# Optimization experiments

Measured on AMD Instinct MI355X. Metric: run time of the kernel, lower is better.

The kernel has to match this reference:

```python
import jax, jax.numpy as jnp
import numpy as np

EPS = 1e-7
BLOCK = 64  # block_size from init_kwargs


def project(x):
    norm = jnp.clip(jnp.linalg.norm(x, axis=-1, keepdims=True), EPS)
    return jnp.where(norm >= 1.0, x / norm * (1.0 - EPS), x)


def mobius_add(x, y, c):
    x2 = jnp.sum(x * x, -1, keepdims=True)
    y2 = jnp.sum(y * y, -1, keepdims=True)
    xy = jnp.sum(x * y, -1, keepdims=True)
    num = (1 + 2 * c * xy + c * y2) * x + (1 - c * x2) * y
    den = 1 + 2 * c * xy + c * c * x2 * y2
    return project(num / jnp.clip(den, EPS))


def logmap0(y, c):
    sqrt_c = jnp.clip(jnp.sqrt(c), EPS)
    yn = jnp.linalg.norm(y, axis=-1, keepdims=True)
    mag = jnp.arctanh(jnp.minimum(yn, 1.0 - EPS)) / sqrt_c
    return jnp.where(yn < EPS, jnp.zeros_like(y), mag * (y / jnp.clip(yn, EPS)))


def expmap0(v, c):
    sqrt_c = jnp.clip(jnp.sqrt(c), EPS)
    vn = jnp.linalg.norm(v, axis=-1, keepdims=True)
    mag = jnp.tanh(sqrt_c * jnp.clip(vn, EPS)) / sqrt_c
    return project(jnp.where(vn < EPS, jnp.zeros_like(v), mag * (v / jnp.clip(vn, EPS))))


def pdist(x, y, c):
    # x: [B,H,S,1,D], y: [B,H,1,S,D], c: [1,H,1,1,1] -> [B,H,S,S]
    sqrt_c = jnp.clip(jnp.sqrt(c), EPS)
    add_norm = jnp.linalg.norm(mobius_add(-x, y, c), axis=-1)
    sc = jnp.squeeze(sqrt_c, -1)
    arg = jnp.minimum(sc * add_norm, 1.0 - EPS)
    return 2.0 * jnp.arctanh(arg) / sc


def layernorm(x, scale, bias, eps=1e-6):
    mu = jnp.mean(x, -1, keepdims=True)
    var = jnp.mean(jnp.square(x - mu), -1, keepdims=True)
    return (x - mu) * jax.lax.rsqrt(var + eps) * scale + bias


def precompute_freqs_cis(dim, end, theta=10000.0):
    f = 1.0 / theta ** (jnp.arange(0, dim, 2, dtype=jnp.float32) / dim)
    return jnp.exp(1j * jnp.outer(jnp.arange(end), f))


def rope(x, fc):
    # split-half rotary, as in WubuBlock.apply_rotary_emb
    xr, xi = jnp.split(x, 2, -1)
    xc = jax.lax.complex(xr, xi) * fc.reshape(1, 1, fc.shape[0], fc.shape[1])
    return jnp.concatenate([xc.real, xc.imag], -1)


def setup_inputs() -> dict:
    key = jax.random.key(0)
    ks = jax.random.split(key, 8)
    B, N, D, H = 1, 1024, 512, 8
    w = lambda k, shape, s=0.02: jax.random.normal(k, shape, jnp.float32) * s
    return {
        'x': w(ks[0], (B, N, D), 0.02),  # points well inside the Poincare ball
        'c_global': jax.random.uniform(ks[1], (B, 1), jnp.float32, 0.5, 1.5),
        'W_qkv': w(ks[2], (D, 3 * D)), 'b_qkv': jnp.zeros((3 * D,), jnp.float32),
        'W_out': w(ks[3], (D, D)), 'b_out': jnp.zeros((D,), jnp.float32),
        'ln1_scale': jnp.ones((D,), jnp.float32), 'ln1_bias': jnp.zeros((D,), jnp.float32),
        'ln2_scale': jnp.ones((D,), jnp.float32), 'ln2_bias': jnp.zeros((D,), jnp.float32),
        'W_ff1': w(ks[4], (D, 4 * D)), 'b_ff1': jnp.zeros((4 * D,), jnp.float32),
        'W_ff2': w(ks[5], (4 * D, D)), 'b_ff2': jnp.zeros((D,), jnp.float32),
        'c_per_head_logits': jnp.zeros((H,), jnp.float32),
        'geo_scale': jnp.ones((1, H, 1, 1), jnp.float32),
        'start_pos': 0,
    }


def reference(x, c_global, W_qkv, b_qkv, W_out, b_out, ln1_scale, ln1_bias,
              ln2_scale, ln2_bias, W_ff1, b_ff1, W_ff2, b_ff2,
              c_per_head_logits, geo_scale, start_pos):
    B, N, D = x.shape
    H = c_per_head_logits.shape[0]
    hd = D // H
    S = BLOCK
    nb = N // S
    Be = B * nb
    xb = x.reshape(Be, S, D)
    c_b = jnp.repeat(c_global, nb, axis=0).reshape(Be, 1, 1)

    # tangent-space layernorm (norm1) then logmap to tangent for QKV proj
    xn = expmap0(layernorm(logmap0(xb, c_b), ln1_scale, ln1_bias), c_b)
    xt = logmap0(xn, c_b)
    qkv = (xt @ W_qkv + b_qkv).reshape(Be, S, 3, H, hd).transpose(2, 0, 3, 1, 4)
    q, k, v = qkv[0], qkv[1], qkv[2]  # [Be,H,S,hd]

    fc = precompute_freqs_cis(hd, S)
    q = rope(q, fc)
    k = rope(k, fc)

    c_h = jax.nn.softplus(c_per_head_logits).reshape(1, H, 1, 1)
    qh = expmap0(q, c_h)
    kh = expmap0(k, c_h)

    # full pairwise hyperbolic distance: [Be,H,S,S]
    d = pdist(qh[:, :, :, None, :], kh[:, :, None, :, :], c_h[:, :, None, :, :])
    attn = jax.nn.softmax(-geo_scale * d, axis=-1)
    ao = jnp.einsum('bhqk,bhkd->bhqd', attn, v)
    ao = ao.transpose(0, 2, 1, 3).reshape(Be, S, D)

    ah = expmap0(ao @ W_out + b_out, c_b)
    xa = mobius_add(xb, ah, c_b)  # hyperbolic residual

    # hyperbolic FFN with tangent-space norm (norm2)
    xn2 = expmap0(layernorm(logmap0(xa, c_b), ln2_scale, ln2_bias), c_b)
    t = logmap0(xn2, c_b)
    fh = expmap0(jax.nn.gelu(t @ W_ff1 + b_ff1) @ W_ff2 + b_ff2, c_b)
    out = mobius_add(xa, fh, c_b)
    return out.reshape(B, N, D)
```

## Files before the change

kernel.cpp:

```cpp
#include <hip/hip_runtime.h>
#include <math.h>

#define DEV __device__ __forceinline__
typedef _Float16 h16;
typedef __attribute__((ext_vector_type(8))) _Float16 h8v;
typedef __attribute__((ext_vector_type(4))) _Float16 h4v;
typedef __attribute__((ext_vector_type(4))) float f4v;

constexpr int NTOK = 1024;
constexpr int D    = 512;
constexpr int H    = 8;
constexpr int NB   = 16;
constexpr double EPSd = 1e-7;

DEV double wave_sum(double v) {
#pragma unroll
  for (int m = 32; m; m >>= 1) v += __shfl_xor(v, m, 64);
  return v;
}

DEV void tcast64(const float* __restrict__ src, h16* __restrict__ dst,
                 int K, int N, int n0, int k0, float* tls ) {
  const int tx = threadIdx.x & 15, ty = threadIdx.x >> 4;
#pragma unroll
  for (int it = 0; it < 4; ++it) {
    const int k = ty + it * 16;
    float4 v = *(const float4*)(src + (size_t)(k0 + k) * N + n0 + tx * 4);
    *(float4*)(tls + k * 68 + tx * 4) = v;
  }
  __syncthreads();
#pragma unroll
  for (int it = 0; it < 4; ++it) {
    const int n = ty + it * 16;
    const int kc = tx * 4;
    h4v o;
#pragma unroll
    for (int j = 0; j < 4; ++j) o[j] = (h16)tls[(kc + j) * 68 + n];
    *(h4v*)(dst + (size_t)(n0 + n) * K + k0 + kc) = o;
  }
}

__global__ void k_prep(const float* __restrict__ Wqkv,
                       const float* __restrict__ x, const float* __restrict__ cg,
                       const float* __restrict__ s1, const float* __restrict__ b1,
                       h16* __restrict__ qT, h16* __restrict__ xt) {
  __shared__ __align__(16) float tls[64 * 68];
  const int bid = blockIdx.x;
  if (bid < 192) {
    tcast64(Wqkv, qT, 512, 1536, (bid % 24) * 64, (bid / 24) * 64, tls);
    return;
  }
  const int wid = threadIdx.x >> 6, lane = threadIdx.x & 63;
  const int tok = (bid - 192) * 4 + wid;
  const float4* xr = (const float4*)(x + (size_t)tok * D);
  float4 xv0 = xr[lane], xv1 = xr[lane + 64];
  double sv = 0.0, svv = 0.0;
  {
    const float e[8] = {xv0.x, xv0.y, xv0.z, xv0.w, xv1.x, xv1.y, xv1.z, xv1.w};
#pragma unroll
    for (int j = 0; j < 8; ++j) { double d = e[j]; sv += d; svv += d * d; }
  }
  sv = wave_sum(sv); svv = wave_sum(svv);
  double c = (double)cg[0];
  double sc = sqrt(c); if (sc < EPSd) sc = EPSd;
  double yn = sqrt(svv);
  double arg0 = yn; if (arg0 > 1.0 - EPSd) arg0 = 1.0 - EPSd;
  double f = (yn < EPSd) ? 0.0 : atanh(arg0) / sc / fmax(yn, EPSd);
  double mu = f * sv / D;
  double var = f * f * svv / D - mu * mu;
  double rs = 1.0 / sqrt(var + 1e-6);
  const float4* s1r = (const float4*)s1;
  const float4* b1r = (const float4*)b1;
  float4 sA = s1r[lane], sB = s1r[lane + 64];
  float4 bA = b1r[lane], bB = b1r[lane + 64];
  double w[8]; double sww = 0.0;
  {
    const float e[8]  = {xv0.x, xv0.y, xv0.z, xv0.w, xv1.x, xv1.y, xv1.z, xv1.w};
    const float se[8] = {sA.x, sA.y, sA.z, sA.w, sB.x, sB.y, sB.z, sB.w};
    const float be[8] = {bA.x, bA.y, bA.z, bA.w, bB.x, bB.y, bB.z, bB.w};
#pragma unroll
    for (int j = 0; j < 8; ++j) {
      w[j] = (f * (double)e[j] - mu) * rs * (double)se[j] + (double)be[j];
      sww += w[j] * w[j];
    }
  }
  sww = wave_sum(sww);
  double vn = sqrt(sww);
  double F = 0.0;
  if (vn >= EPSd) {
    double mag_e = tanh(sc * fmax(vn, EPSd)) / sc;
    F = atanh(fmin(mag_e, 1.0 - EPSd)) / (sc * vn);
  }
  h16* dst = xt + (size_t)tok * D;
#pragma unroll
  for (int half = 0; half < 2; ++half) {
    h4v o;
#pragma unroll
    for (int e = 0; e < 4; ++e) o[e] = (h16)(float)(F * w[half * 4 + e]);
    *(h4v*)(dst + 4 * (lane + 64 * half)) = o;
  }
}

DEV void stage_tile(const h16* __restrict__ gbase, int rowstride, h16* lds,
                    int wid, int lane) {
#pragma unroll
  for (int j = 0; j < 2; ++j) {
    const int rbase = wid * 16 + j * 8;
    const int grow = rbase + (lane >> 3);
    const int gch = (lane & 7) ^ (lane >> 3);
    const h16* gp = gbase + (size_t)grow * rowstride + gch * 8;
    __builtin_amdgcn_global_load_lds(
        (const __attribute__((address_space(1))) void*)gp,
        (__attribute__((address_space(3))) void*)(lds + rbase * 64), 16, 0, 0);
  }
}
DEV h8v read_frag(const h16* lds, int row, int c) {
  const int p = c ^ (row & 7);
  return *(const h8v*)(lds + row * 64 + p * 8);
}

template <int GELU, int OHALF, int SPLITK>
__global__ __launch_bounds__(256) void k_mm(
    const h16* __restrict__ A, const h16* __restrict__ B,
    const float* __restrict__ bias, float* __restrict__ Cf, h16* __restrict__ Ch,
    int M, int N, int K) {
  __shared__ __align__(16) h16 As[3][64 * 64];
  __shared__ __align__(16) h16 Bs[3][64 * 64];
  const int tid = threadIdx.x;
  const int lane = tid & 63, wid = tid >> 6;
  const int wr = (wid >> 1) * 32, wc = (wid & 1) * 32;
  const int lr = lane & 15, lg = lane >> 4;
  const size_t r0 = (size_t)blockIdx.y * 64, c0 = (size_t)blockIdx.x * 64;
  const int kz = SPLITK ? blockIdx.z : 0;
  const int Keff = SPLITK ? (K >> 1) : K;
  const f4v z = {0.f, 0.f, 0.f, 0.f};
  f4v acc[2][2]; acc[0][0] = z; acc[0][1] = z; acc[1][0] = z; acc[1][1] = z;
  const h16* Abase = A + r0 * K + (size_t)kz * Keff;
  const h16* Bbase = B + c0 * K + (size_t)kz * Keff;
  const int NT = Keff >> 6;
  const size_t col0 = c0 + wc + lr;
  float bv0 = bias[col0];
  float bv1 = bias[col0 + 16];
  asm volatile("" :: "v"(bv0), "v"(bv1));
  asm volatile("s_waitcnt vmcnt(0)" ::: "memory");
  if (SPLITK && kz) { bv0 = 0.f; bv1 = 0.f; }
  stage_tile(Abase, K, As[0], wid, lane);
  stage_tile(Bbase, K, Bs[0], wid, lane);
  stage_tile(Abase + 64, K, As[1], wid, lane);
  stage_tile(Bbase + 64, K, Bs[1], wid, lane);
  int cur = 0;
  for (int t = 0; t < NT; ++t) {
    const int pre = (cur == 2) ? 0 : cur + 1;
    const int pre2 = (pre == 2) ? 0 : pre + 1;
    if (t + 2 < NT) {
      stage_tile(Abase + (t + 2) * 64, K, As[pre2], wid, lane);
      stage_tile(Bbase + (t + 2) * 64, K, Bs[pre2], wid, lane);
    }
    const int rem = NT - 1 - t;
    if (rem >= 2)      asm volatile("s_waitcnt vmcnt(8)" ::: "memory");
    else if (rem == 1) asm volatile("s_waitcnt vmcnt(4)" ::: "memory");
    else               asm volatile("s_waitcnt vmcnt(0)" ::: "memory");
    asm volatile("s_barrier" ::: "memory");
    const h16* Ac = As[cur];
    const h16* Bc = Bs[cur];
#pragma unroll
    for (int ks = 0; ks < 2; ++ks) {
      const int c = ks * 4 + lg;
      h8v a0 = read_frag(Ac, wr + lr, c);
      h8v a1 = read_frag(Ac, wr + 16 + lr, c);
      h8v b0 = read_frag(Bc, wc + lr, c);
      h8v b1 = read_frag(Bc, wc + 16 + lr, c);
      acc[0][0] = __builtin_amdgcn_mfma_f32_16x16x32_f16(a0, b0, acc[0][0], 0, 0, 0);
      acc[0][1] = __builtin_amdgcn_mfma_f32_16x16x32_f16(a0, b1, acc[0][1], 0, 0, 0);
      acc[1][0] = __builtin_amdgcn_mfma_f32_16x16x32_f16(a1, b0, acc[1][0], 0, 0, 0);
      acc[1][1] = __builtin_amdgcn_mfma_f32_16x16x32_f16(a1, b1, acc[1][1], 0, 0, 0);
    }
    asm volatile("s_barrier" ::: "memory");
    cur = pre;
  }
  float* Cfo = Cf + (size_t)kz * M * N;
#pragma unroll
  for (int m = 0; m < 2; ++m)
#pragma unroll
    for (int n = 0; n < 2; ++n) {
      const size_t row = r0 + wr + m * 16 + lg * 4;
      const size_t col = col0 + n * 16;
      const float bv = n ? bv1 : bv0;
#pragma unroll
      for (int e = 0; e < 4; ++e) {
        float v = acc[m][n][e] + bv;
        if (GELU) {
          float x3 = v * v * v;
          v = 0.5f * v * (1.0f + tanhf(0.7978845608028654f * (v + 0.044715f * x3)));
        }
        if (OHALF) Ch[(row + e) * N + col] = (h16)v;
        else       Cfo[(row + e) * N + col] = v;
      }
    }
}

__global__ __launch_bounds__(256) void k_attn(
    const h16* __restrict__ qkv, const float* __restrict__ chl,
    const float* __restrict__ geo, h16* __restrict__ ao,
    const float* __restrict__ Wo, const float* __restrict__ Wf1,
    const float* __restrict__ Wf2,
    h16* __restrict__ oT, h16* __restrict__ f1T, h16* __restrict__ f2T) {
  __shared__ __align__(16) float Qs[32][68];
  __shared__ __align__(16) float Kt[64][68];
  __shared__ __align__(16) float Vs[64][68];
  __shared__ float q2raw[32], k2raw[64];
  __shared__ float q2s[32], k2s[64], fqv[32], fkv[64];
  const int bid = blockIdx.x;
  if (bid >= 256) {
    const float* src; h16* dst; int K, N, bx, by, l;
    if (bid < 320)      { l = bid - 256; src = Wo;  dst = oT;  K = 512;  N = 512;  bx = l % 8;  by = l / 8;  }
    else if (bid < 576) { l = bid - 320; src = Wf1; dst = f1T; K = 512;  N = 2048; bx = l % 32; by = l / 32; }
    else                { l = bid - 576; src = Wf2; dst = f2T; K = 2048; N = 512;  bx = l % 8;  by = l / 8;  }
    tcast64(src, dst, K, N, bx * 64, by * 64, &Kt[0][0]);
    return;
  }
  const int be = bid >> 4, h = (bid >> 1) & 7, q0 = (bid & 1) * 32;
  const int tid = threadIdx.x;
  const double chd = log1p(exp((double)chl[h]));
  const float ch = (float)chd;
  float sc = (float)sqrt(chd); if (sc < 1e-7f) sc = 1e-7f;
  {
    const int s = tid >> 2, jc = (tid & 3) * 8;
    const h16* base = qkv + (size_t)(be * 64 + s) * 1536 + h * 64;
    h8v klo = *(const h8v*)(base + 512 + jc);
    h8v khi = *(const h8v*)(base + 512 + jc + 32);
    h8v vlo = *(const h8v*)(base + 1024 + jc);
    h8v vhi = *(const h8v*)(base + 1024 + jc + 32);
    float racc = 0.f;
#pragma unroll
    for (int j = 0; j < 8; ++j) {
      float ka = (float)klo[j], kb = (float)khi[j];
      racc += ka * ka + kb * kb;
      float fj = expf((float)(jc + j) * -0.2878231366242557f);
      float st, ct; sincosf((float)s * fj, &st, &ct);
      Kt[jc + j][s]      = ka * ct - kb * st;
      Kt[jc + j + 32][s] = ka * st + kb * ct;
    }
    float4 v0, v1;
#pragma unroll
    for (int j = 0; j < 4; ++j) { v0[j] = (float)vlo[j]; v1[j] = (float)vlo[j + 4]; }
    *(float4*)&Vs[s][jc] = v0; *(float4*)&Vs[s][jc + 4] = v1;
#pragma unroll
    for (int j = 0; j < 4; ++j) { v0[j] = (float)vhi[j]; v1[j] = (float)vhi[j + 4]; }
    *(float4*)&Vs[s][jc + 32] = v0; *(float4*)&Vs[s][jc + 36] = v1;
    racc += __shfl_xor(racc, 1, 64);
    racc += __shfl_xor(racc, 2, 64);
    if ((tid & 3) == 0) k2raw[s] = racc;
  }
  if (tid < 128) {
    const int s = tid >> 2, jc = (tid & 3) * 8;
    const h16* base = qkv + (size_t)(be * 64 + q0 + s) * 1536 + h * 64;
    h8v qlo = *(const h8v*)(base + jc);
    h8v qhi = *(const h8v*)(base + jc + 32);
    float racc = 0.f;
    float rl[8], rh[8];
#pragma unroll
    for (int j = 0; j < 8; ++j) {
      float qa = (float)qlo[j], qb = (float)qhi[j];
      racc += qa * qa + qb * qb;
      float fj = expf((float)(jc + j) * -0.2878231366242557f);
      float st, ct; sincosf((float)(q0 + s) * fj, &st, &ct);
      rl[j] = qa * ct - qb * st;
      rh[j] = qa * st + qb * ct;
    }
    *(float4*)&Qs[s][jc]      = {rl[0], rl[1], rl[2], rl[3]};
    *(float4*)&Qs[s][jc + 4]  = {rl[4], rl[5], rl[6], rl[7]};
    *(float4*)&Qs[s][jc + 32] = {rh[0], rh[1], rh[2], rh[3]};
    *(float4*)&Qs[s][jc + 36] = {rh[4], rh[5], rh[6], rh[7]};
    racc += __shfl_xor(racc, 1, 64);
    racc += __shfl_xor(racc, 2, 64);
    if ((tid & 3) == 0) q2raw[s] = racc;
  }
  __syncthreads();
  if (tid < 64) {
    float n = sqrtf(k2raw[tid]);
    float m = tanhf(sc * fmaxf(n, 1e-7f)) / sc;
    float f = (n < 1e-7f) ? 0.f : m / fmaxf(n, 1e-7f);
    if (m >= 1.f) f *= (1.f - 1e-7f) / m;
    float fn = f * n;
    fkv[tid] = f; k2s[tid] = fn * fn;
  } else if (tid < 96) {
    int i = tid - 64;
    float n = sqrtf(q2raw[i]);
    float m = tanhf(sc * fmaxf(n, 1e-7f)) / sc;
    float f = (n < 1e-7f) ? 0.f : m / fmaxf(n, 1e-7f);
    if (m >= 1.f) f *= (1.f - 1e-7f) / m;
    float fn = f * n;
    fqv[i] = f; q2s[i] = fn * fn;
  }
  __syncthreads();
  const int i = tid >> 3, g = tid & 7;
  float gacc[8];
#pragma unroll
  for (int jj = 0; jj < 8; ++jj) gacc[jj] = 0.f;
  for (int d2 = 0; d2 < 64; ++d2) {
    float qv = Qs[i][d2];
    const float4* kp = (const float4*)&Kt[d2][g * 8];
    float4 k0 = kp[0], k1 = kp[1];
    gacc[0] += qv * k0.x; gacc[1] += qv * k0.y; gacc[2] += qv * k0.z; gacc[3] += qv * k0.w;
    gacc[4] += qv * k1.x; gacc[5] += qv * k1.y; gacc[6] += qv * k1.z; gacc[7] += qv * k1.w;
  }
  const float gs = geo[h];
  const float q2 = q2s[i], fqi = fqv[i];
  float lg[8];
  float mx = -1e30f;
#pragma unroll
  for (int jj = 0; jj < 8; ++jj) {
    float gq = fqi * fkv[g * 8 + jj] * gacc[jj];
    float k2 = k2s[g * 8 + jj];
    float A  = 1.f - 2.f * ch * gq + ch * k2;
    float Bv = 1.f - ch * q2;
    float n2 = fmaxf(A * A * q2 - 2.f * A * Bv * gq + Bv * Bv * k2, 0.f);
    float den = fmaxf(1.f - 2.f * ch * gq + ch * ch * q2 * k2, 1e-7f);
    float r = fminf(sqrtf(n2) / den, 1.f - 1e-7f);
    float arg = fminf(sc * r, 1.f - 1e-7f);
    float l = -gs * (2.f * atanhf(arg) / sc);
    lg[jj] = l; mx = fmaxf(mx, l);
  }
  mx = fmaxf(mx, __shfl_xor(mx, 1, 64));
  mx = fmaxf(mx, __shfl_xor(mx, 2, 64));
  mx = fmaxf(mx, __shfl_xor(mx, 4, 64));
  float pv[8]; float sum = 0.f;
#pragma unroll
  for (int jj = 0; jj < 8; ++jj) { pv[jj] = expf(lg[jj] - mx); sum += pv[jj]; }
  sum += __shfl_xor(sum, 1, 64);
  sum += __shfl_xor(sum, 2, 64);
  sum += __shfl_xor(sum, 4, 64);
  float inv = 1.0f / sum;
#pragma unroll
  for (int jj = 0; jj < 8; ++jj) Qs[i][g * 8 + jj] = pv[jj] * inv;
  float oacc[8];
#pragma unroll
  for (int dd = 0; dd < 8; ++dd) oacc[dd] = 0.f;
  for (int jv = 0; jv < 64; ++jv) {
    float p = Qs[i][jv];
    const float4* vp = (const float4*)&Vs[jv][g * 8];
    float4 v0 = vp[0], v1 = vp[1];
    oacc[0] += p * v0.x; oacc[1] += p * v0.y; oacc[2] += p * v0.z; oacc[3] += p * v0.w;
    oacc[4] += p * v1.x; oacc[5] += p * v1.y; oacc[6] += p * v1.z; oacc[7] += p * v1.w;
  }
  h8v ov;
#pragma unroll
  for (int dd = 0; dd < 8; ++dd) ov[dd] = (h16)oacc[dd];
  *(h8v*)(ao + (size_t)(be * 64 + q0 + i) * D + h * 64 + g * 8) = ov;
}

__global__ void k_resid(const float* __restrict__ x, const float* __restrict__ proj,
                        const float* __restrict__ cg, const float* __restrict__ s2,
                        const float* __restrict__ b2, float* __restrict__ xa,
                        h16* __restrict__ t2) {
  const int wid = threadIdx.x >> 6, lane = threadIdx.x & 63;
  const int tok = blockIdx.x * 4 + wid;
  const float4* xr  = (const float4*)(x + (size_t)tok * D);
  const float4* p0r = (const float4*)(proj + (size_t)tok * D);
  const float4* p1r = (const float4*)(proj + (size_t)NTOK * D + (size_t)tok * D);
  float4 xv0 = xr[lane], xv1 = xr[lane + 64];
  float4 pa0 = p0r[lane], pa1 = p0r[lane + 64];
  float4 pb0 = p1r[lane], pb1 = p1r[lane + 64];
  float pe[8], xe[8];
  xe[0]=xv0.x; xe[1]=xv0.y; xe[2]=xv0.z; xe[3]=xv0.w; xe[4]=xv1.x; xe[5]=xv1.y; xe[6]=xv1.z; xe[7]=xv1.w;
  pe[0]=pa0.x+pb0.x; pe[1]=pa0.y+pb0.y; pe[2]=pa0.z+pb0.z; pe[3]=pa0.w+pb0.w;
  pe[4]=pa1.x+pb1.x; pe[5]=pa1.y+pb1.y; pe[6]=pa1.z+pb1.z; pe[7]=pa1.w+pb1.w;
  double sx = 0, sp = 0, xx = 0, pp = 0, xp = 0;
#pragma unroll
  for (int j = 0; j < 8; ++j) {
    double dx = xe[j], dp = pe[j];
    sx += dx; sp += dp; xx += dx * dx; pp += dp * dp; xp += dx * dp;
  }
  sx = wave_sum(sx); sp = wave_sum(sp); xx = wave_sum(xx);
  pp = wave_sum(pp); xp = wave_sum(xp);
  double c = (double)cg[0];
  double sc = sqrt(c); if (sc < EPSd) sc = EPSd;
  double pn = sqrt(pp);
  double me = tanh(sc * fmax(pn, EPSd)) / sc;
  double fs = (pn < EPSd) ? 0.0 : me / fmax(pn, EPSd);
  if (me >= 1.0) fs *= (1.0 - EPSd) / me;
  double y2 = fs * fs * pp, xy = fs * xp;
  double a = 1.0 + 2.0 * c * xy + c * y2;
  double b = 1.0 - c * xx;
  double den = 1.0 + 2.0 * c * xy + c * c * xx * y2;
  if (den < EPSd) den = EPSd;
  double zn = sqrt(fmax(a * a * xx + 2.0 * a * b * xy + b * b * y2, 0.0)) / den;
  double zs = 1.0 / den;
  if (zn >= 1.0) zs *= (1.0 - EPSd) / zn;
  double xan = (zn >= 1.0) ? (1.0 - EPSd) : zn;
  double A0 = zs * a, B0 = zs * b * fs;
  double xav[8];
#pragma unroll
  for (int j = 0; j < 8; ++j) xav[j] = A0 * (double)xe[j] + B0 * (double)pe[j];
  {
    float4 o0 = {(float)xav[0], (float)xav[1], (float)xav[2], (float)xav[3]};
    float4 o1 = {(float)xav[4], (float)xav[5], (float)xav[6], (float)xav[7]};
    float4* xw = (float4*)(xa + (size_t)tok * D);
    xw[lane] = o0; xw[lane + 64] = o1;
  }
  double sxa  = A0 * sx + B0 * sp;
  double sxa2 = A0 * A0 * xx + 2.0 * A0 * B0 * xp + B0 * B0 * pp;
  double fl = 0.0;
  if (xan >= EPSd) fl = atanh(fmin(xan, 1.0 - EPSd)) / (sc * fmax(xan, EPSd));
  double mu = fl * sxa / D;
  double var = fl * fl * sxa2 / D - mu * mu;
  double rs = 1.0 / sqrt(var + 1e-6);
  const float4* s2r = (const float4*)s2;
  const float4* b2r = (const float4*)b2;
  float4 sA = s2r[lane], sB = s2r[lane + 64];
  float4 bA = b2r[lane], bB = b2r[lane + 64];
  const float se[8] = {sA.x, sA.y, sA.z, sA.w, sB.x, sB.y, sB.z, sB.w};
  const float be[8] = {bA.x, bA.y, bA.z, bA.w, bB.x, bB.y, bB.z, bB.w};
  double w[8]; double sww = 0.0;
#pragma unroll
  for (int j = 0; j < 8; ++j) {
    w[j] = (fl * xav[j] - mu) * rs * (double)se[j] + (double)be[j];
    sww += w[j] * w[j];
  }
  sww = wave_sum(sww);
  double vn = sqrt(sww);
  double F = 0.0;
  if (vn >= EPSd) {
    double mag_e = tanh(sc * fmax(vn, EPSd)) / sc;
    F = atanh(fmin(mag_e, 1.0 - EPSd)) / (sc * vn);
  }
  h16* dst = t2 + (size_t)tok * D;
#pragma unroll
  for (int half = 0; half < 2; ++half) {
    h4v o;
#pragma unroll
    for (int e = 0; e < 4; ++e) o[e] = (h16)(float)(F * w[half * 4 + e]);
    *(h4v*)(dst + 4 * (lane + 64 * half)) = o;
  }
}

__global__ void k_final(const float* __restrict__ xa, const float* __restrict__ f2,
                        const float* __restrict__ cg, float* __restrict__ out) {
  const int wid = threadIdx.x >> 6, lane = threadIdx.x & 63;
  const int tok = blockIdx.x * 4 + wid;
  const float4* ar  = (const float4*)(xa + (size_t)tok * D);
  const float4* f0r = (const float4*)(f2 + (size_t)tok * D);
  const float4* f1r = (const float4*)(f2 + (size_t)NTOK * D + (size_t)tok * D);
  float4 xv0 = ar[lane], xv1 = ar[lane + 64];
  float4 pa0 = f0r[lane], pa1 = f0r[lane + 64];
  float4 pb0 = f1r[lane], pb1 = f1r[lane + 64];
  float pe[8], xe[8];
  xe[0]=xv0.x; xe[1]=xv0.y; xe[2]=xv0.z; xe[3]=xv0.w; xe[4]=xv1.x; xe[5]=xv1.y; xe[6]=xv1.z; xe[7]=xv1.w;
  pe[0]=pa0.x+pb0.x; pe[1]=pa0.y+pb0.y; pe[2]=pa0.z+pb0.z; pe[3]=pa0.w+pb0.w;
  pe[4]=pa1.x+pb1.x; pe[5]=pa1.y+pb1.y; pe[6]=pa1.z+pb1.z; pe[7]=pa1.w+pb1.w;
  double xx = 0, pp = 0, xp = 0;
#pragma unroll
  for (int j = 0; j < 8; ++j) {
    double dx = xe[j], dp = pe[j];
    xx += dx * dx; pp += dp * dp; xp += dx * dp;
  }
  xx = wave_sum(xx); pp = wave_sum(pp); xp = wave_sum(xp);
  double c = (double)cg[0];
  double sc = sqrt(c); if (sc < EPSd) sc = EPSd;
  double pn = sqrt(pp);
  double me = tanh(sc * fmax(pn, EPSd)) / sc;
  double fs = (pn < EPSd) ? 0.0 : me / fmax(pn, EPSd);
  if (me >= 1.0) fs *= (1.0 - EPSd) / me;
  double y2 = fs * fs * pp, xy = fs * xp;
  double a = 1.0 + 2.0 * c * xy + c * y2;
  double b = 1.0 - c * xx;
  double den = 1.0 + 2.0 * c * xy + c * c * xx * y2;
  if (den < EPSd) den = EPSd;
  double zn = sqrt(fmax(a * a * xx + 2.0 * a * b * xy + b * b * y2, 0.0)) / den;
  double zs = 1.0 / den;
  if (zn >= 1.0) zs *= (1.0 - EPSd) / zn;
  double A0 = zs * a, B0 = zs * b * fs;
  float4 o0, o1;
  o0.x = (float)(A0 * xe[0] + B0 * pe[0]); o0.y = (float)(A0 * xe[1] + B0 * pe[1]);
  o0.z = (float)(A0 * xe[2] + B0 * pe[2]); o0.w = (float)(A0 * xe[3] + B0 * pe[3]);
  o1.x = (float)(A0 * xe[4] + B0 * pe[4]); o1.y = (float)(A0 * xe[5] + B0 * pe[5]);
  o1.z = (float)(A0 * xe[6] + B0 * pe[6]); o1.w = (float)(A0 * xe[7] + B0 * pe[7]);
  float4* ow = (float4*)(out + (size_t)tok * D);
  ow[lane] = o0; ow[lane + 64] = o1;
}

extern "C" void kernel_launch(void* const* d_in, const int* in_sizes, int n_in,
                              void* d_out, int out_size, void* d_ws, size_t ws_size,
                              hipStream_t stream) {
  (void)in_sizes; (void)n_in; (void)out_size; (void)ws_size;
  const float* x    = (const float*)d_in[0];
  const float* cg   = (const float*)d_in[1];
  const float* Wqkv = (const float*)d_in[2];
  const float* bqkv = (const float*)d_in[3];
  const float* Wout = (const float*)d_in[4];
  const float* bout = (const float*)d_in[5];
  const float* s1   = (const float*)d_in[6];
  const float* b1   = (const float*)d_in[7];
  const float* s2   = (const float*)d_in[8];
  const float* b2   = (const float*)d_in[9];
  const float* Wff1 = (const float*)d_in[10];
  const float* bff1 = (const float*)d_in[11];
  const float* Wff2 = (const float*)d_in[12];
  const float* bff2 = (const float*)d_in[13];
  const float* chl  = (const float*)d_in[14];
  const float* geo  = (const float*)d_in[15];
  float* out = (float*)d_out;

  char* base = (char*)d_ws;
  const size_t MB = 1024 * 1024;
  h16*   WqkvT = (h16*)(base + 0);
  h16*   WoutT = (h16*)(base + (3*MB)/2);
  h16*   Wff1T = (h16*)(base + 2*MB);
  h16*   Wff2T = (h16*)(base + 4*MB);
  h16*   xt    = (h16*)(base + 6*MB);
  h16*   qkv   = (h16*)(base + 7*MB);
  h16*   ao    = (h16*)(base + 10*MB);
  float* proj  = (float*)(base + 11*MB);
  float* xa    = (float*)(base + 7*MB);
  h16*   t2    = (h16*)(base + 6*MB);
  h16*   h1    = (h16*)(base + 11*MB);
  float* f2    = (float*)(base + 0);

  k_prep<<<192 + NTOK / 4, 256, 0, stream>>>(Wqkv, x, cg, s1, b1, WqkvT, xt);
  k_mm<0, 1, 0><<<dim3(1536 / 64, NTOK / 64), 256, 0, stream>>>(
      xt, WqkvT, bqkv, nullptr, qkv, NTOK, 1536, 512);
  k_attn<<<NB * H * 2 + 576, 256, 0, stream>>>(qkv, chl, geo, ao,
                                               Wout, Wff1, Wff2, WoutT, Wff1T, Wff2T);
  k_mm<0, 0, 1><<<dim3(512 / 64, NTOK / 64, 2), 256, 0, stream>>>(
      ao, WoutT, bout, proj, nullptr, NTOK, 512, 512);
  k_resid<<<NTOK / 4, 256, 0, stream>>>(x, proj, cg, s2, b2, xa, t2);
  k_mm<1, 1, 0><<<dim3(2048 / 64, NTOK / 64), 256, 0, stream>>>(
      t2, Wff1T, bff1, nullptr, h1, NTOK, 2048, 512);
  k_mm<0, 0, 1><<<dim3(512 / 64, NTOK / 64, 2), 256, 0, stream>>>(
      h1, Wff2T, bff2, f2, nullptr, NTOK, 512, 2048);
  k_final<<<NTOK / 4, 256, 0, stream>>>(xa, f2, cg, out);
}
```

Baseline: 68.38 us.

## Fuse all stages into one persistent cooperative kernel with grid syncs

Replaces the eight separate kernel launches with a single cooperative kernel of 256 blocks. Each stage loops over its work tiles and is separated from the next by grid.sync(). All weight transposes move into the first stage, so the attention kernel no longer carries the Wout/Wff1/Wff2 transposes. The aim is to remove launch overhead and inter-kernel gaps. In exchange, every stage is capped at 256 blocks, grid barriers add their own cost, and shared memory is a fixed 48KB pool reused by every stage.

```diff
diff --git a/kernel.cpp b/kernel.cpp
--- a/kernel.cpp
+++ b/kernel.cpp
@@ -1,5 +1,8 @@
 #include <hip/hip_runtime.h>
+#include <hip/hip_cooperative_groups.h>
 #include <math.h>
+
+namespace cg = cooperative_groups;
 
 #define DEV __device__ __forceinline__
 typedef _Float16 h16;
@@ -9,9 +12,15 @@
 
 constexpr int NTOK = 1024;
 constexpr int D    = 512;
-constexpr int H    = 8;
-constexpr int NB   = 16;
 constexpr double EPSd = 1e-7;
+
+struct KParams {
+  const float *x, *cgl, *Wqkv, *bqkv, *Wout, *bout, *s1, *b1, *s2, *b2;
+  const float *Wff1, *bff1, *Wff2, *bff2, *chl, *geo;
+  float* out;
+  h16 *WqkvT, *WoutT, *Wff1T, *Wff2T, *xt, *qkv, *ao, *t2, *h1;
+  float *proj, *xa, *f2;
+};
 
 DEV double wave_sum(double v) {
 #pragma unroll
@@ -40,19 +49,10 @@
   }
 }
 
-__global__ void k_prep(const float* __restrict__ Wqkv,
-                       const float* __restrict__ x, const float* __restrict__ cg,
-                       const float* __restrict__ s1, const float* __restrict__ b1,
-                       h16* __restrict__ qT, h16* __restrict__ xt) {
-  __shared__ __align__(16) float tls[64 * 68];
-  const int bid = blockIdx.x;
-  if (bid < 192) {
-    tcast64(Wqkv, qT, 512, 1536, (bid % 24) * 64, (bid / 24) * 64, tls);
-    return;
-  }
+DEV void do_pre(int pb, const KParams& p) {
   const int wid = threadIdx.x >> 6, lane = threadIdx.x & 63;
-  const int tok = (bid - 192) * 4 + wid;
-  const float4* xr = (const float4*)(x + (size_t)tok * D);
+  const int tok = pb * 4 + wid;
+  const float4* xr = (const float4*)(p.x + (size_t)tok * D);
   float4 xv0 = xr[lane], xv1 = xr[lane + 64];
   double sv = 0.0, svv = 0.0;
   {
@@ -61,7 +61,7 @@
     for (int j = 0; j < 8; ++j) { double d = e[j]; sv += d; svv += d * d; }
   }
   sv = wave_sum(sv); svv = wave_sum(svv);
-  double c = (double)cg[0];
+  double c = (double)p.cgl[0];
   double sc = sqrt(c); if (sc < EPSd) sc = EPSd;
   double yn = sqrt(svv);
   double arg0 = yn; if (arg0 > 1.0 - EPSd) arg0 = 1.0 - EPSd;
@@ -69,8 +69,8 @@
   double mu = f * sv / D;
   double var = f * f * svv / D - mu * mu;
   double rs = 1.0 / sqrt(var + 1e-6);
-  const float4* s1r = (const float4*)s1;
-  const float4* b1r = (const float4*)b1;
+  const float4* s1r = (const float4*)p.s1;
+  const float4* b1r = (const float4*)p.b1;
   float4 sA = s1r[lane], sB = s1r[lane + 64];
   float4 bA = b1r[lane], bB = b1r[lane + 64];
   double w[8]; double sww = 0.0;
@@ -91,7 +91,7 @@
     double mag_e = tanh(sc * fmax(vn, EPSd)) / sc;
     F = atanh(fmin(mag_e, 1.0 - EPSd)) / (sc * vn);
   }
-  h16* dst = xt + (size_t)tok * D;
+  h16* dst = p.xt + (size_t)tok * D;
 #pragma unroll
   for (int half = 0; half < 2; ++half) {
     h4v o;
@@ -120,18 +120,15 @@
 }
 
 template <int GELU, int OHALF, int SPLITK>
-__global__ __launch_bounds__(256) void k_mm(
-    const h16* __restrict__ A, const h16* __restrict__ B,
-    const float* __restrict__ bias, float* __restrict__ Cf, h16* __restrict__ Ch,
-    int M, int N, int K) {
-  __shared__ __align__(16) h16 As[3][64 * 64];
-  __shared__ __align__(16) h16 Bs[3][64 * 64];
+DEV void mm_body(h16* AsB, h16* BsB,
+                 const h16* __restrict__ A, const h16* __restrict__ B,
+                 const float* __restrict__ bias, float* __restrict__ Cf,
+                 h16* __restrict__ Ch, int M, int N, int K, int bxx, int byy, int kz) {
   const int tid = threadIdx.x;
   const int lane = tid & 63, wid = tid >> 6;
   const int wr = (wid >> 1) * 32, wc = (wid & 1) * 32;
   const int lr = lane & 15, lg = lane >> 4;
-  const size_t r0 = (size_t)blockIdx.y * 64, c0 = (size_t)blockIdx.x * 64;
-  const int kz = SPLITK ? blockIdx.z : 0;
+  const size_t r0 = (size_t)byy * 64, c0 = (size_t)bxx * 64;
   const int Keff = SPLITK ? (K >> 1) : K;
   const f4v z = {0.f, 0.f, 0.f, 0.f};
   f4v acc[2][2]; acc[0][0] = z; acc[0][1] = z; acc[1][0] = z; acc[1][1] = z;
@@ -144,25 +141,25 @@
   asm volatile("" :: "v"(bv0), "v"(bv1));
   asm volatile("s_waitcnt vmcnt(0)" ::: "memory");
   if (SPLITK && kz) { bv0 = 0.f; bv1 = 0.f; }
-  stage_tile(Abase, K, As[0], wid, lane);
-  stage_tile(Bbase, K, Bs[0], wid, lane);
-  stage_tile(Abase + 64, K, As[1], wid, lane);
-  stage_tile(Bbase + 64, K, Bs[1], wid, lane);
+  stage_tile(Abase, K, AsB, wid, lane);
+  stage_tile(Bbase, K, BsB, wid, lane);
+  stage_tile(Abase + 64, K, AsB + 4096, wid, lane);
+  stage_tile(Bbase + 64, K, BsB + 4096, wid, lane);
   int cur = 0;
   for (int t = 0; t < NT; ++t) {
     const int pre = (cur == 2) ? 0 : cur + 1;
     const int pre2 = (pre == 2) ? 0 : pre + 1;
     if (t + 2 < NT) {
-      stage_tile(Abase + (t + 2) * 64, K, As[pre2], wid, lane);
-      stage_tile(Bbase + (t + 2) * 64, K, Bs[pre2], wid, lane);
+      stage_tile(Abase + (t + 2) * 64, K, AsB + pre2 * 4096, wid, lane);
+      stage_tile(Bbase + (t + 2) * 64, K, BsB + pre2 * 4096, wid, lane);
     }
     const int rem = NT - 1 - t;
     if (rem >= 2)      asm volatile("s_waitcnt vmcnt(8)" ::: "memory");
     else if (rem == 1) asm volatile("s_waitcnt vmcnt(4)" ::: "memory");
     else               asm volatile("s_waitcnt vmcnt(0)" ::: "memory");
     asm volatile("s_barrier" ::: "memory");
-    const h16* Ac = As[cur];
-    const h16* Bc = Bs[cur];
+    const h16* Ac = AsB + cur * 4096;
+    const h16* Bc = BsB + cur * 4096;
 #pragma unroll
     for (int ks = 0; ks < 2; ++ks) {
       const int c = ks * 4 + lg;
@@ -199,34 +196,25 @@
     }
 }
 
-__global__ __launch_bounds__(256) void k_attn(
-    const h16* __restrict__ qkv, const float* __restrict__ chl,
-    const float* __restrict__ geo, h16* __restrict__ ao,
-    const float* __restrict__ Wo, const float* __restrict__ Wf1,
-    const float* __restrict__ Wf2,
-    h16* __restrict__ oT, h16* __restrict__ f1T, h16* __restrict__ f2T) {
-  __shared__ __align__(16) float Qs[32][68];
-  __shared__ __align__(16) float Kt[64][68];
-  __shared__ __align__(16) float Vs[64][68];
-  __shared__ float q2raw[32], k2raw[64];
-  __shared__ float q2s[32], k2s[64], fqv[32], fkv[64];
-  const int bid = blockIdx.x;
-  if (bid >= 256) {
-    const float* src; h16* dst; int K, N, bx, by, l;
-    if (bid < 320)      { l = bid - 256; src = Wo;  dst = oT;  K = 512;  N = 512;  bx = l % 8;  by = l / 8;  }
-    else if (bid < 576) { l = bid - 320; src = Wf1; dst = f1T; K = 512;  N = 2048; bx = l % 32; by = l / 32; }
-    else                { l = bid - 576; src = Wf2; dst = f2T; K = 2048; N = 512;  bx = l % 8;  by = l / 8;  }
-    tcast64(src, dst, K, N, bx * 64, by * 64, &Kt[0][0]);
-    return;
-  }
+DEV void do_attn(int bid, const KParams& p, char* SM) {
+  float (*Qs)[68] = (float(*)[68])SM;
+  float (*Kt)[68] = (float(*)[68])(SM + 8704);
+  float (*Vs)[68] = (float(*)[68])(SM + 26112);
+  float* q2raw = (float*)(SM + 43520);
+  float* k2raw = (float*)(SM + 43648);
+  float* q2s   = (float*)(SM + 43904);
+  float* k2s   = (float*)(SM + 44032);
+  float* fqv   = (float*)(SM + 44288);
+  float* fkv   = (float*)(SM + 44416);
   const int be = bid >> 4, h = (bid >> 1) & 7, q0 = (bid & 1) * 32;
   const int tid = threadIdx.x;
-  const double chd = log1p(exp((double)chl[h]));
+  const double chd = log1p(exp((double)p.chl[h]));
   const float ch = (float)chd;
   float sc = (float)sqrt(chd); if (sc < 1e-7f) sc = 1e-7f;
+  __syncthreads();
   {
     const int s = tid >> 2, jc = (tid & 3) * 8;
-    const h16* base = qkv + (size_t)(be * 64 + s) * 1536 + h * 64;
+    const h16* base = p.qkv + (size_t)(be * 64 + s) * 1536 + h * 64;
     h8v klo = *(const h8v*)(base + 512 + jc);
     h8v khi = *(const h8v*)(base + 512 + jc + 32);
     h8v vlo = *(const h8v*)(base + 1024 + jc);
@@ -254,7 +242,7 @@
   }
   if (tid < 128) {
     const int s = tid >> 2, jc = (tid & 3) * 8;
-    const h16* base = qkv + (size_t)(be * 64 + q0 + s) * 1536 + h * 64;
+    const h16* base = p.qkv + (size_t)(be * 64 + q0 + s) * 1536 + h * 64;
     h8v qlo = *(const h8v*)(base + jc);
     h8v qhi = *(const h8v*)(base + jc + 32);
     float racc = 0.f;
@@ -305,7 +293,7 @@
     gacc[0] += qv * k0.x; gacc[1] += qv * k0.y; gacc[2] += qv * k0.z; gacc[3] += qv * k0.w;
     gacc[4] += qv * k1.x; gacc[5] += qv * k1.y; gacc[6] += qv * k1.z; gacc[7] += qv * k1.w;
   }
-  const float gs = geo[h];
+  const float gs = p.geo[h];
   const float q2 = q2s[i], fqi = fqv[i];
   float lg[8];
   float mx = -1e30f;
@@ -338,27 +326,24 @@
 #pragma unroll
   for (int dd = 0; dd < 8; ++dd) oacc[dd] = 0.f;
   for (int jv = 0; jv < 64; ++jv) {
-    float p = Qs[i][jv];
+    float ppv = Qs[i][jv];
     const float4* vp = (const float4*)&Vs[jv][g * 8];
     float4 v0 = vp[0], v1 = vp[1];
-    oacc[0] += p * v0.x; oacc[1] += p * v0.y; oacc[2] += p * v0.z; oacc[3] += p * v0.w;
-    oacc[4] += p * v1.x; oacc[5] += p * v1.y; oacc[6] += p * v1.z; oacc[7] += p * v1.w;
+    oacc[0] += ppv * v0.x; oacc[1] += ppv * v0.y; oacc[2] += ppv * v0.z; oacc[3] += ppv * v0.w;
+    oacc[4] += ppv * v1.x; oacc[5] += ppv * v1.y; oacc[6] += ppv * v1.z; oacc[7] += ppv * v1.w;
   }
   h8v ov;
 #pragma unroll
   for (int dd = 0; dd < 8; ++dd) ov[dd] = (h16)oacc[dd];
-  *(h8v*)(ao + (size_t)(be * 64 + q0 + i) * D + h * 64 + g * 8) = ov;
-}
-
-__global__ void k_resid(const float* __restrict__ x, const float* __restrict__ proj,
-                        const float* __restrict__ cg, const float* __restrict__ s2,
-                        const float* __restrict__ b2, float* __restrict__ xa,
-                        h16* __restrict__ t2) {
+  *(h8v*)(p.ao + (size_t)(be * 64 + q0 + i) * D + h * 64 + g * 8) = ov;
+}
+
+DEV void do_resid(int pb, const KParams& p) {
   const int wid = threadIdx.x >> 6, lane = threadIdx.x & 63;
-  const int tok = blockIdx.x * 4 + wid;
-  const float4* xr  = (const float4*)(x + (size_t)tok * D);
-  const float4* p0r = (const float4*)(proj + (size_t)tok * D);
-  const float4* p1r = (const float4*)(proj + (size_t)NTOK * D + (size_t)tok * D);
+  const int tok = pb * 4 + wid;
+  const float4* xr  = (const float4*)(p.x + (size_t)tok * D);
+  const float4* p0r = (const float4*)(p.proj + (size_t)tok * D);
+  const float4* p1r = (const float4*)(p.proj + (size_t)NTOK * D + (size_t)tok * D);
   float4 xv0 = xr[lane], xv1 = xr[lane + 64];
   float4 pa0 = p0r[lane], pa1 = p0r[lane + 64];
   float4 pb0 = p1r[lane], pb1 = p1r[lane + 64];
@@ -374,7 +359,7 @@
   }
   sx = wave_sum(sx); sp = wave_sum(sp); xx = wave_sum(xx);
   pp = wave_sum(pp); xp = wave_sum(xp);
-  double c = (double)cg[0];
+  double c = (double)p.cgl[0];
   double sc = sqrt(c); if (sc < EPSd) sc = EPSd;
   double pn = sqrt(pp);
   double me = tanh(sc * fmax(pn, EPSd)) / sc;
@@ -396,7 +381,7 @@
   {
     float4 o0 = {(float)xav[0], (float)xav[1], (float)xav[2], (float)xav[3]};
     float4 o1 = {(float)xav[4], (float)xav[5], (float)xav[6], (float)xav[7]};
-    float4* xw = (float4*)(xa + (size_t)tok * D);
+    float4* xw = (float4*)(p.xa + (size_t)tok * D);
     xw[lane] = o0; xw[lane + 64] = o1;
   }
   double sxa  = A0 * sx + B0 * sp;
@@ -406,8 +391,8 @@
   double mu = fl * sxa / D;
   double var = fl * fl * sxa2 / D - mu * mu;
   double rs = 1.0 / sqrt(var + 1e-6);
-  const float4* s2r = (const float4*)s2;
-  const float4* b2r = (const float4*)b2;
+  const float4* s2r = (const float4*)p.s2;
+  const float4* b2r = (const float4*)p.b2;
   float4 sA = s2r[lane], sB = s2r[lane + 64];
   float4 bA = b2r[lane], bB = b2r[lane + 64];
   const float se[8] = {sA.x, sA.y, sA.z, sA.w, sB.x, sB.y, sB.z, sB.w};
@@ -425,7 +410,7 @@
     double mag_e = tanh(sc * fmax(vn, EPSd)) / sc;
     F = atanh(fmin(mag_e, 1.0 - EPSd)) / (sc * vn);
   }
-  h16* dst = t2 + (size_t)tok * D;
+  h16* dst = p.t2 + (size_t)tok * D;
 #pragma unroll
   for (int half = 0; half < 2; ++half) {
     h4v o;
@@ -435,13 +420,12 @@
   }
 }
 
-__global__ void k_final(const float* __restrict__ xa, const float* __restrict__ f2,
-                        const float* __restrict__ cg, float* __restrict__ out) {
+DEV void do_final(int pb, const KParams& p) {
   const int wid = threadIdx.x >> 6, lane = threadIdx.x & 63;
-  const int tok = blockIdx.x * 4 + wid;
-  const float4* ar  = (const float4*)(xa + (size_t)tok * D);
-  const float4* f0r = (const float4*)(f2 + (size_t)tok * D);
-  const float4* f1r = (const float4*)(f2 + (size_t)NTOK * D + (size_t)tok * D);
+  const int tok = pb * 4 + wid;
+  const float4* ar  = (const float4*)(p.xa + (size_t)tok * D);
+  const float4* f0r = (const float4*)(p.f2 + (size_t)tok * D);
+  const float4* f1r = (const float4*)(p.f2 + (size_t)NTOK * D + (size_t)tok * D);
   float4 xv0 = ar[lane], xv1 = ar[lane + 64];
   float4 pa0 = f0r[lane], pa1 = f0r[lane + 64];
   float4 pb0 = f1r[lane], pb1 = f1r[lane + 64];
@@ -456,7 +440,7 @@
     xx += dx * dx; pp += dp * dp; xp += dx * dp;
   }
   xx = wave_sum(xx); pp = wave_sum(pp); xp = wave_sum(xp);
-  double c = (double)cg[0];
+  double c = (double)p.cgl[0];
   double sc = sqrt(c); if (sc < EPSd) sc = EPSd;
   double pn = sqrt(pp);
   double me = tanh(sc * fmax(pn, EPSd)) / sc;
@@ -476,58 +460,88 @@
   o0.z = (float)(A0 * xe[2] + B0 * pe[2]); o0.w = (float)(A0 * xe[3] + B0 * pe[3]);
   o1.x = (float)(A0 * xe[4] + B0 * pe[4]); o1.y = (float)(A0 * xe[5] + B0 * pe[5]);
   o1.z = (float)(A0 * xe[6] + B0 * pe[6]); o1.w = (float)(A0 * xe[7] + B0 * pe[7]);
-  float4* ow = (float4*)(out + (size_t)tok * D);
+  float4* ow = (float4*)(p.out + (size_t)tok * D);
   ow[lane] = o0; ow[lane + 64] = o1;
+}
+
+__global__ __launch_bounds__(256, 2) void k_all(KParams p) {
+  __shared__ __align__(16) char SM[49152];
+  cg::grid_group grid = cg::this_grid();
+  const int nb = gridDim.x;
+  for (int t = blockIdx.x; t < 1024; t += nb) {
+    __syncthreads();
+    if (t < 768) {
+      const float* src; h16* dst; int K, N, bx, by, l;
+      if (t < 192)      { l = t;       src = p.Wqkv; dst = p.WqkvT; K = 512;  N = 1536; bx = l % 24; by = l / 24; }
+      else if (t < 256) { l = t - 192; src = p.Wout; dst = p.WoutT; K = 512;  N = 512;  bx = l % 8;  by = l / 8;  }
+      else if (t < 512) { l = t - 256; src = p.Wff1; dst = p.Wff1T; K = 512;  N = 2048; bx = l % 32; by = l / 32; }
+      else              { l = t - 512; src = p.Wff2; dst = p.Wff2T; K = 2048; N = 512;  bx = l % 8;  by = l / 8;  }
+      tcast64(src, dst, K, N, bx * 64, by * 64, (float*)SM);
+    } else {
+      do_pre(t - 768, p);
+    }
+  }
+  grid.sync();
+  for (int t = blockIdx.x; t < 384; t += nb)
+    mm_body<0, 1, 0>((h16*)SM, (h16*)(SM + 24576), p.xt, p.WqkvT, p.bqkv,
+                     nullptr, p.qkv, NTOK, 1536, 512, t % 24, t / 24, 0);
+  grid.sync();
+  for (int t = blockIdx.x; t < 256; t += nb) do_attn(t, p, SM);
+  grid.sync();
+  for (int t = blockIdx.x; t < 256; t += nb)
+    mm_body<0, 0, 1>((h16*)SM, (h16*)(SM + 24576), p.ao, p.WoutT, p.bout,
+                     p.proj, nullptr, NTOK, 512, 512, t % 8, (t >> 3) & 15, t >> 7);
+  grid.sync();
+  for (int t = blockIdx.x; t < 256; t += nb) do_resid(t, p);
+  grid.sync();
+  for (int t = blockIdx.x; t < 512; t += nb)
+    mm_body<1, 1, 0>((h16*)SM, (h16*)(SM + 24576), p.t2, p.Wff1T, p.bff1,
+                     nullptr, p.h1, NTOK, 2048, 512, t % 32, t / 32, 0);
+  grid.sync();
+  for (int t = blockIdx.x; t < 256; t += nb)
+    mm_body<0, 0, 1>((h16*)SM, (h16*)(SM + 24576), p.h1, p.Wff2T, p.bff2,
+                     p.f2, nullptr, NTOK, 512, 2048, t % 8, (t >> 3) & 15, t >> 7);
+  grid.sync();
+  for (int t = blockIdx.x; t < 256; t += nb) do_final(t, p);
 }
 
 extern "C" void kernel_launch(void* const* d_in, const int* in_sizes, int n_in,
                               void* d_out, int out_size, void* d_ws, size_t ws_size,
                               hipStream_t stream) {
   (void)in_sizes; (void)n_in; (void)out_size; (void)ws_size;
-  const float* x    = (const float*)d_in[0];
-  const float* cg   = (const float*)d_in[1];
-  const float* Wqkv = (const float*)d_in[2];
-  const float* bqkv = (const float*)d_in[3];
-  const float* Wout = (const float*)d_in[4];
-  const float* bout = (const float*)d_in[5];
-  const float* s1   = (const float*)d_in[6];
-  const float* b1   = (const float*)d_in[7];
-  const float* s2   = (const float*)d_in[8];
-  const float* b2   = (const float*)d_in[9];
-  const float* Wff1 = (const float*)d_in[10];
-  const float* bff1 = (const float*)d_in[11];
-  const float* Wff2 = (const float*)d_in[12];
-  const float* bff2 = (const float*)d_in[13];
-  const float* chl  = (const float*)d_in[14];
-  const float* geo  = (const float*)d_in[15];
-  float* out = (float*)d_out;
-
   char* base = (char*)d_ws;
   const size_t MB = 1024 * 1024;
-  h16*   WqkvT = (h16*)(base + 0);
-  h16*   WoutT = (h16*)(base + (3*MB)/2);
-  h16*   Wff1T = (h16*)(base + 2*MB);
-  h16*   Wff2T = (h16*)(base + 4*MB);
-  h16*   xt    = (h16*)(base + 6*MB);
-  h16*   qkv   = (h16*)(base + 7*MB);
-  h16*   ao    = (h16*)(base + 10*MB);
-  float* proj  = (float*)(base + 11*MB);
-  float* xa    = (float*)(base + 7*MB);
-  h16*   t2    = (h16*)(base + 6*MB);
-  h16*   h1    = (h16*)(base + 11*MB);
-  float* f2    = (float*)(base + 0);
-
-  k_prep<<<192 + NTOK / 4, 256, 0, stream>>>(Wqkv, x, cg, s1, b1, WqkvT, xt);
-  k_mm<0, 1, 0><<<dim3(1536 / 64, NTOK / 64), 256, 0, stream>>>(
-      xt, WqkvT, bqkv, nullptr, qkv, NTOK, 1536, 512);
-  k_attn<<<NB * H * 2 + 576, 256, 0, stream>>>(qkv, chl, geo, ao,
-                                               Wout, Wff1, Wff2, WoutT, Wff1T, Wff2T);
-  k_mm<0, 0, 1><<<dim3(512 / 64, NTOK / 64, 2), 256, 0, stream>>>(
-      ao, WoutT, bout, proj, nullptr, NTOK, 512, 512);
-  k_resid<<<NTOK / 4, 256, 0, stream>>>(x, proj, cg, s2, b2, xa, t2);
-  k_mm<1, 1, 0><<<dim3(2048 / 64, NTOK / 64), 256, 0, stream>>>(
-      t2, Wff1T, bff1, nullptr, h1, NTOK, 2048, 512);
-  k_mm<0, 0, 1><<<dim3(512 / 64, NTOK / 64, 2), 256, 0, stream>>>(
-      h1, Wff2T, bff2, f2, nullptr, NTOK, 512, 2048);
-  k_final<<<NTOK / 4, 256, 0, stream>>>(xa, f2, cg, out);
-}
+  KParams p;
+  p.x    = (const float*)d_in[0];
+  p.cgl  = (const float*)d_in[1];
+  p.Wqkv = (const float*)d_in[2];
+  p.bqkv = (const float*)d_in[3];
+  p.Wout = (const float*)d_in[4];
+  p.bout = (const float*)d_in[5];
+  p.s1   = (const float*)d_in[6];
+  p.b1   = (const float*)d_in[7];
+  p.s2   = (const float*)d_in[8];
+  p.b2   = (const float*)d_in[9];
+  p.Wff1 = (const float*)d_in[10];
+  p.bff1 = (const float*)d_in[11];
+  p.Wff2 = (const float*)d_in[12];
+  p.bff2 = (const float*)d_in[13];
+  p.chl  = (const float*)d_in[14];
+  p.geo  = (const float*)d_in[15];
+  p.out  = (float*)d_out;
+  p.WqkvT = (h16*)(base + 0);
+  p.WoutT = (h16*)(base + (3 * MB) / 2);
+  p.Wff1T = (h16*)(base + 2 * MB);
+  p.Wff2T = (h16*)(base + 4 * MB);
+  p.xt    = (h16*)(base + 6 * MB);
+  p.qkv   = (h16*)(base + 7 * MB);
+  p.ao    = (h16*)(base + 10 * MB);
+  p.proj  = (float*)(base + 11 * MB);
+  p.xa    = (float*)(base + 7 * MB);
+  p.t2    = (h16*)(base + 6 * MB);
+  p.h1    = (h16*)(base + 11 * MB);
+  p.f2    = (float*)(base + 0);
+
+  void* args[] = {&p};
+  hipLaunchCooperativeKernel((void*)k_all, dim3(256), dim3(256), args, 0, stream);
+}
```

Result: slower. 255.1 us (+273.0%).
